# Kernel tuning notes

Measured on AMD Instinct MI355X. Metric: run time of the kernel, lower is better.

## Reference

```python
import jax, jax.numpy as jnp
import numpy as np

B, S, D, H, DK, F = 4, 2048, 1024, 16, 64, 4096


def layer_norm(x, g, b, eps=1e-5):
    mu = jnp.mean(x, axis=-1, keepdims=True)
    var = jnp.var(x, axis=-1, keepdims=True)
    return (x - mu) * jax.lax.rsqrt(var + eps) * g + b


def setup_inputs() -> dict:
    key = jax.random.key(0)
    ks = jax.random.split(key, 16)
    s = 0.02
    return {
        "src": jax.random.normal(ks[0], (B, S, D), jnp.float32),
        # per-head q/k/v projections stacked over heads: (H, D, DK)
        "Wq": jax.random.normal(ks[1], (H, D, DK), jnp.float32) * s,
        "bq": jnp.zeros((H, DK), jnp.float32),
        "Wk": jax.random.normal(ks[2], (H, D, DK), jnp.float32) * s,
        "bk": jnp.zeros((H, DK), jnp.float32),
        "Wv": jax.random.normal(ks[3], (H, D, DK), jnp.float32) * s,
        "bv": jnp.zeros((H, DK), jnp.float32),
        "Wo": jax.random.normal(ks[4], (H * DK, D), jnp.float32) * s,
        "bo": jnp.zeros((D,), jnp.float32),
        "ln1_g": jnp.ones((D,), jnp.float32),
        "ln1_b": jnp.zeros((D,), jnp.float32),
        "W1": jax.random.normal(ks[5], (D, F), jnp.float32) * s,
        "b1": jnp.zeros((F,), jnp.float32),
        "W2": jax.random.normal(ks[6], (F, D), jnp.float32) * s,
        "b2": jnp.zeros((D,), jnp.float32),
        "ln2_g": jnp.ones((D,), jnp.float32),
        "ln2_b": jnp.zeros((D,), jnp.float32),
    }


def reference(src, Wq, bq, Wk, bk, Wv, bv, Wo, bo, ln1_g, ln1_b, W1, b1, W2, b2, ln2_g, ln2_b):
    # --- multi-head attention (all heads batched via einsum) ---
    q = jnp.einsum("bsd,hdk->bhsk", src, Wq) + bq[None, :, None, :]
    k = jnp.einsum("bsd,hdk->bhsk", src, Wk) + bk[None, :, None, :]
    v = jnp.einsum("bsd,hdk->bhsk", src, Wv) + bv[None, :, None, :]
    scale = jnp.sqrt(jnp.asarray(DK, q.dtype))
    scores = jnp.einsum("bhqk,bhsk->bhqs", q, k) / scale  # [B,H,S,S]
    p = jax.nn.softmax(scores, axis=-1)
    ctx = jnp.einsum("bhqs,bhsk->bhqk", p, v)             # [B,H,S,DK]
    ctx = ctx.transpose(0, 2, 1, 3).reshape(src.shape[0], src.shape[1], H * DK)
    attn_out = ctx @ Wo + bo
    x = layer_norm(src + attn_out, ln1_g, ln1_b)
    # --- feed-forward ---
    ff = jax.nn.relu(x @ W1 + b1) @ W2 + b2
    return layer_norm(x + ff, ln2_g, ln2_b)
```

## Files before the change

### kernel.cpp

```cpp
#include <hip/hip_runtime.h>
#include <hip/hip_bf16.h>
#include <cstddef>
#include <cstdint>

typedef __bf16 bf16;
typedef __bf16 bf16x4 __attribute__((ext_vector_type(4)));
typedef __bf16 bf16x8 __attribute__((ext_vector_type(8)));
typedef float f32x4 __attribute__((ext_vector_type(4)));
typedef float f32x16 __attribute__((ext_vector_type(16)));
typedef unsigned int u32x4 __attribute__((ext_vector_type(4)));

#define GLD_LDS16(g, l) __builtin_amdgcn_global_load_lds( \
    (const __attribute__((address_space(1))) void*)(g),   \
    (__attribute__((address_space(3))) void*)(l), 16, 0, 0)

static __device__ inline unsigned int cvtpk(float lo, float hi) {
  unsigned int r;
  asm("v_cvt_pk_bf16_f32 %0, %1, %2" : "=v"(r) : "v"(lo), "v"(hi));
  return r;
}
static __device__ inline void plswap(unsigned int& a, unsigned int& b) {
  asm("v_permlane32_swap_b32 %0, %1" : "+v"(a), "+v"(b));
}
static __device__ inline float fexp2(float x) {
#if __has_builtin(__builtin_amdgcn_exp2f)
  return __builtin_amdgcn_exp2f(x);
#else
  float r; asm("v_exp_f32 %0, %1" : "=v"(r) : "v"(x)); return r;
#endif
}
static __device__ inline float tsum16(const float* e) {
  float s0 = e[0] + e[1], s1 = e[2] + e[3], s2 = e[4] + e[5], s3 = e[6] + e[7];
  float s4 = e[8] + e[9], s5 = e[10] + e[11], s6 = e[12] + e[13], s7 = e[14] + e[15];
  return ((s0 + s1) + (s2 + s3)) + ((s4 + s5) + (s6 + s7));
}

__global__ void __launch_bounds__(256)
k_cast(const float* __restrict__ in, bf16* __restrict__ out) {
  int gid = blockIdx.x * 256 + threadIdx.x;
  f32x4 a = ((const f32x4*)in)[gid * 2];
  f32x4 b = ((const f32x4*)in)[gid * 2 + 1];
  bf16x8 o;
#pragma unroll
  for (int i = 0; i < 4; ++i) { o[i] = (bf16)a[i]; o[i + 4] = (bf16)b[i]; }
  ((bf16x8*)out)[gid] = o;
}

__global__ void __launch_bounds__(256)
k_transpose_t(const float* __restrict__ in, bf16* __restrict__ out, int R, int C) {
  __shared__ float tile[64][68];
  const int nct = C >> 6;
  const int bc = blockIdx.x % nct, br = blockIdx.x / nct;
  const int r0 = br << 6, c0 = bc << 6;
  const int t = threadIdx.x;
  const int tr = t >> 4, tc4 = (t & 15) << 2;
#pragma unroll
  for (int i = 0; i < 4; ++i)
    *(f32x4*)&tile[i * 16 + tr][tc4] =
        *(const f32x4*)&in[(size_t)(r0 + i * 16 + tr) * C + c0 + tc4];
  __syncthreads();
  const int c = t >> 2, rch = (t & 3) << 4;
  bf16 ob[16];
#pragma unroll
  for (int j = 0; j < 16; ++j) ob[j] = (bf16)tile[rch + j][c];
  bf16* dst = out + (size_t)(c0 + c) * R + r0 + rch;
  *(bf16x8*)&dst[0] = *(bf16x8*)&ob[0];
  *(bf16x8*)&dst[8] = *(bf16x8*)&ob[8];
}

__global__ void __launch_bounds__(256)
k_reorder_qkv_t(const float* __restrict__ Wq, const float* __restrict__ Wk,
                const float* __restrict__ Wv, bf16* __restrict__ WqkvT) {
  __shared__ float tile[64][68];
  const int bid = blockIdx.x;
  const int sub = bid >> 4, tl = bid & 15;
  const int proj = sub >> 4, h = sub & 15;
  const float* W = (proj == 0) ? Wq : (proj == 1) ? Wk : Wv;
  const float* src = W + (size_t)h * 65536;
  const int r0 = tl << 6;
  const int t = threadIdx.x, tr = t >> 4, tc4 = (t & 15) << 2;
#pragma unroll
  for (int i = 0; i < 4; ++i)
    *(f32x4*)&tile[i * 16 + tr][tc4] =
        *(const f32x4*)&src[(size_t)(r0 + i * 16 + tr) * 64 + tc4];
  __syncthreads();
  const int c = t >> 2, rch = (t & 3) << 4;
  bf16 ob[16];
#pragma unroll
  for (int j = 0; j < 16; ++j) ob[j] = (bf16)tile[rch + j][c];
  bf16* dst = WqkvT + ((size_t)(proj * 1024 + h * 64 + c)) * 1024 + r0 + rch;
  *(bf16x8*)&dst[0] = *(bf16x8*)&ob[0];
  *(bf16x8*)&dst[8] = *(bf16x8*)&ob[8];
}

__global__ void __launch_bounds__(256)
k_bias_qkv(const float* __restrict__ bq, const float* __restrict__ bk,
           const float* __restrict__ bv, float* __restrict__ bqkv) {
  int n = blockIdx.x * 256 + threadIdx.x;
  int proj = n >> 10, wi = n & 1023;
  const float* bb = (proj == 0) ? bq : (proj == 1) ? bk : bv;
  bqkv[n] = bb[wi];
}

template <int MODE>
__global__ void __launch_bounds__(256)
k_gemm_bt(const bf16* __restrict__ A, const bf16* __restrict__ Bt,
          const float* __restrict__ bias, void* __restrict__ outp,
          int M, int N, int K,
          bf16* __restrict__ qb, bf16* __restrict__ kb, bf16* __restrict__ vb) {
  __shared__ __align__(16) bf16 As[2][128][32];
  __shared__ __align__(16) bf16 Bs[2][128][32];
  const int tid = threadIdx.x;
  const int wave = tid >> 6, lane = tid & 63;
  const int l16 = lane & 15, lq = lane >> 4;
  const int mtiles = M >> 7;
  const int tile_m = (blockIdx.x % mtiles) << 7;
  const int tile_n = (blockIdx.x / mtiles) << 7;
  const int wm = (wave >> 1) << 6, wn = (wave & 1) << 6;

  const bf16* Arow = A + (size_t)tile_m * K;
  const bf16* Brow = Bt + (size_t)tile_n * K;
  bf16* As_f = &As[0][0][0];
  bf16* Bs_f = &Bs[0][0][0];

  int gA[4], rA[4], kA[4];
#pragma unroll
  for (int j = 0; j < 4; ++j) {
    gA[j] = j * 4 + wave;
    rA[j] = (gA[j] & 7) * 16 + (lane >> 2);
    kA[j] = (gA[j] >> 3) * 32 + (lane & 3) * 8;
  }

  f32x4 acc[4][4] = {};

  for (int k0 = 0; k0 < K; k0 += 64) {
    __syncthreads();
#pragma unroll
    for (int j = 0; j < 4; ++j) {
      GLD_LDS16(Arow + (size_t)rA[j] * K + k0 + kA[j], As_f + gA[j] * 512);
      GLD_LDS16(Brow + (size_t)rA[j] * K + k0 + kA[j], Bs_f + gA[j] * 512);
    }
    __syncthreads();
#pragma unroll
    for (int p = 0; p < 2; ++p) {
      bf16x8 af[4], bfr[4];
#pragma unroll
      for (int mi = 0; mi < 4; ++mi)
        af[mi] = *(const bf16x8*)&As[p][wm + mi * 16 + l16][lq * 8];
#pragma unroll
      for (int ni = 0; ni < 4; ++ni)
        bfr[ni] = *(const bf16x8*)&Bs[p][wn + ni * 16 + l16][lq * 8];
#pragma unroll
      for (int mi = 0; mi < 4; ++mi)
#pragma unroll
        for (int ni = 0; ni < 4; ++ni)
          acc[mi][ni] = __builtin_amdgcn_mfma_f32_16x16x32_bf16(af[mi], bfr[ni], acc[mi][ni], 0, 0, 0);
    }
  }

#pragma unroll
  for (int mi = 0; mi < 4; ++mi) {
#pragma unroll
    for (int ni = 0; ni < 4; ++ni) {
      const int gn = tile_n + wn + ni * 16 + l16;
      const float bb = bias[gn];
      f32x4 v = acc[mi][ni];
      const int gm0 = tile_m + wm + mi * 16 + lq * 4;
      if (MODE == 0) {
        int proj = gn >> 10, wi = gn & 1023;
        int h = wi >> 6, dk = wi & 63;
        int b = gm0 >> 11, sdx = gm0 & 2047;
        size_t bhs = (size_t)((b << 4) + h);
        if (proj == 0) {
#pragma unroll
          for (int i = 0; i < 4; ++i)
            qb[(bhs * 2048 + sdx + i) * 64 + dk] = (bf16)((v[i] + bb) * 0.18033688f);
        } else if (proj == 1) {
#pragma unroll
          for (int i = 0; i < 4; ++i)
            kb[(bhs * 2048 + sdx + i) * 64 + dk] = (bf16)(v[i] + bb);
        } else {
          bf16x4 pk;
#pragma unroll
          for (int i = 0; i < 4; ++i) pk[i] = (bf16)(v[i] + bb);
          *(bf16x4*)&vb[(bhs * 64 + dk) * 2048 + sdx] = pk;
        }
      } else if (MODE == 1) {
#pragma unroll
        for (int i = 0; i < 4; ++i)
          ((bf16*)outp)[(size_t)(gm0 + i) * N + gn] = (bf16)(v[i] + bb);
      } else {
#pragma unroll
        for (int i = 0; i < 4; ++i)
          ((bf16*)outp)[(size_t)(gm0 + i) * N + gn] = (bf16)fmaxf(v[i] + bb, 0.f);
      }
    }
  }
}

__global__ void __launch_bounds__(256, 2)
k_attn(const bf16* __restrict__ qb, const bf16* __restrict__ kb,
       const bf16* __restrict__ vb, bf16* __restrict__ ctx) {
  __shared__ __align__(16) bf16 KsL[3][4096];
  __shared__ __align__(16) bf16 VsL[3][4096];

  const int bid = blockIdx.x;
  const int wg = (bid & 7) * 64 + (bid >> 3);
  const int bh = wg >> 3, qt = wg & 7;

  const bf16* Qp  = qb + (size_t)bh * 131072 + (size_t)qt * 16384;
  const bf16* Kbh = kb + (size_t)bh * 131072;
  const bf16* Vbh = vb + (size_t)bh * 131072;

  const int tid = threadIdx.x, wave = tid >> 6, lane = tid & 63;
  const int l31 = lane & 31, hi = lane >> 5;

  bf16x8 qfA[4], qfB[4];
  {
    const bf16* qra = Qp + (size_t)(wave * 64 + l31) * 64 + hi * 8;
    const bf16* qrb = qra + 32 * 64;
#pragma unroll
    for (int kd = 0; kd < 4; ++kd) {
      qfA[kd] = *(const bf16x8*)(qra + kd * 16);
      qfB[kd] = *(const bf16x8*)(qrb + kd * 16);
    }
  }

  const int c0 = tid, c1 = tid + 256;
  const int sw0 = ((c0 ^ (c0 >> 3)) & 7) * 8, rw0 = c0 >> 3;
  const int sw1 = ((c1 ^ (c1 >> 3)) & 7) * 8, rw1 = c1 >> 3;
  const int kof0 = rw0 * 64 + sw0, kof1 = rw1 * 64 + sw1;
  const int vof0 = rw0 * 2048 + sw0, vof1 = rw1 * 2048 + sw1;

  const int xr = (hi << 4) ^ ((l31 & 7) << 4);
  const int rb = l31 * 128 + xr;

  f32x16 oA[2] = {}, oB[2] = {};
  float lA = 0.f, lB = 0.f;

#define STAGE_KV(buf, s0)                                             \
  do {                                                                \
    GLD_LDS16(Kbh + (size_t)(s0) * 64 + kof0, &KsL[buf][c0 * 8]);     \
    GLD_LDS16(Kbh + (size_t)(s0) * 64 + kof1, &KsL[buf][c1 * 8]);     \
    GLD_LDS16(Vbh + (s0) + vof0, &VsL[buf][c0 * 8]);                  \
    GLD_LDS16(Vbh + (s0) + vof1, &VsL[buf][c1 * 8]);                  \
  } while (0)

  STAGE_KV(0, 0);
  STAGE_KV(1, 64);

  int cur = 0;
  for (int kt = 0; kt < 32; ++kt) {
    __builtin_amdgcn_sched_barrier(0);
    if (kt == 31) { asm volatile("s_waitcnt vmcnt(0)" ::: "memory"); }
    else          { asm volatile("s_waitcnt vmcnt(4)" ::: "memory"); }
    __builtin_amdgcn_s_barrier();
    __builtin_amdgcn_sched_barrier(0);

    if (kt < 30) {
      int nx = cur + 2; if (nx >= 3) nx -= 3;
      STAGE_KV(nx, (kt + 2) * 64);
    }

    const char* Kc = (const char*)&KsL[cur][0];
    const char* Vc = (const char*)&VsL[cur][0];

    bf16x8 paA[4], paB[4];
#pragma unroll
    for (int st = 0; st < 2; ++st) {
      f32x16 sA = {}, sB = {};
      __builtin_amdgcn_s_setprio(1);
#pragma unroll
      for (int kd = 0; kd < 4; ++kd) {
        bf16x8 a = *(const bf16x8*)(Kc + st * 4096 + (rb ^ (kd << 5)));
        sA = __builtin_amdgcn_mfma_f32_32x32x16_bf16(a, qfA[kd], sA, 0, 0, 0);
        sB = __builtin_amdgcn_mfma_f32_32x32x16_bf16(a, qfB[kd], sB, 0, 0, 0);
      }
      __builtin_amdgcn_s_setprio(0);

      float eA[16], eB[16];
#pragma unroll
      for (int i = 0; i < 16; ++i) {
        eA[i] = fexp2(sA[i]);
        eB[i] = fexp2(sB[i]);
      }
      lA += tsum16(eA);
      lB += tsum16(eB);
      unsigned int qdA[4][2], qdB[4][2];
#pragma unroll
      for (int g = 0; g < 4; ++g)
#pragma unroll
        for (int w = 0; w < 2; ++w) {
          qdA[g][w] = cvtpk(eA[g * 4 + w * 2], eA[g * 4 + w * 2 + 1]);
          qdB[g][w] = cvtpk(eB[g * 4 + w * 2], eB[g * 4 + w * 2 + 1]);
        }
#pragma unroll
      for (int a2 = 0; a2 < 2; ++a2) {
        unsigned int x0 = qdA[2 * a2][0], y0 = qdA[2 * a2 + 1][0];
        unsigned int x1 = qdA[2 * a2][1], y1 = qdA[2 * a2 + 1][1];
        plswap(x0, y0); plswap(x1, y1);
        u32x4 fA = {x0, x1, y0, y1};
        paA[st * 2 + a2] = __builtin_bit_cast(bf16x8, fA);
        unsigned int u0 = qdB[2 * a2][0], v0 = qdB[2 * a2 + 1][0];
        unsigned int u1 = qdB[2 * a2][1], v1 = qdB[2 * a2 + 1][1];
        plswap(u0, v0); plswap(u1, v1);
        u32x4 fB = {u0, u1, v0, v1};
        paB[st * 2 + a2] = __builtin_bit_cast(bf16x8, fB);
      }
    }

    __builtin_amdgcn_s_setprio(1);
#pragma unroll
    for (int nd = 0; nd < 2; ++nd)
#pragma unroll
      for (int ks = 0; ks < 4; ++ks) {
        bf16x8 vf = *(const bf16x8*)(Vc + nd * 4096 + (rb ^ (ks << 5)));
        oA[nd] = __builtin_amdgcn_mfma_f32_32x32x16_bf16(paA[ks], vf, oA[nd], 0, 0, 0);
        oB[nd] = __builtin_amdgcn_mfma_f32_32x32x16_bf16(paB[ks], vf, oB[nd], 0, 0, 0);
      }
    __builtin_amdgcn_s_setprio(0);

    if (++cur == 3) cur = 0;
  }
#undef STAGE_KV

  const float ltA = lA + __shfl_xor(lA, 32);
  const float ltB = lB + __shfl_xor(lB, 32);
  const float ivA = 1.f / ltA;
  const float ivB = 1.f / ltB;

  const int b = bh >> 4, h = bh & 15;
  const size_t rowbase = (size_t)(b * 2048 + qt * 256 + wave * 64);
#pragma unroll
  for (int r = 0; r < 16; ++r) {
    const int qr = (r & 3) + 8 * (r >> 2) + 4 * hi;
    const float dA = __shfl(ivA, qr);
    const float dB = __shfl(ivB, qr);
#pragma unroll
    for (int nd = 0; nd < 2; ++nd) {
      const int dk = nd * 32 + l31;
      ctx[(rowbase + qr) * 1024 + h * 64 + dk]      = (bf16)(oA[nd][r] * dA);
      ctx[(rowbase + 32 + qr) * 1024 + h * 64 + dk] = (bf16)(oB[nd][r] * dB);
    }
  }
}

template <typename RT, typename DT, typename OT>
__global__ void __launch_bounds__(256)
k_ln(const RT* __restrict__ resid, const DT* __restrict__ delta,
     const float* __restrict__ g, const float* __restrict__ bta,
     OT* __restrict__ out) {
  const int row = blockIdx.x, tid = threadIdx.x;
  const int wave = tid >> 6, lane = tid & 63;
  __shared__ float rs_[4], rs2_[4];
  const RT* r = resid + (size_t)row * 1024;
  const DT* d = delta + (size_t)row * 1024;
  OT* o = out + (size_t)row * 1024;
  float x[4], s = 0.f, s2 = 0.f;
#pragma unroll
  for (int j = 0; j < 4; ++j) {
    int idx = tid + j * 256;
    float v = (float)r[idx] + (float)d[idx];
    x[j] = v; s += v; s2 += v * v;
  }
#pragma unroll
  for (int m = 32; m >= 1; m >>= 1) { s += __shfl_xor(s, m); s2 += __shfl_xor(s2, m); }
  if (lane == 0) { rs_[wave] = s; rs2_[wave] = s2; }
  __syncthreads();
  float ts = rs_[0] + rs_[1] + rs_[2] + rs_[3];
  float ts2 = rs2_[0] + rs2_[1] + rs2_[2] + rs2_[3];
  float mean = ts * (1.f / 1024.f);
  float var = ts2 * (1.f / 1024.f) - mean * mean;
  float rstd = rsqrtf(var + 1e-5f);
#pragma unroll
  for (int j = 0; j < 4; ++j) {
    int idx = tid + j * 256;
    o[idx] = (OT)((x[j] - mean) * rstd * g[idx] + bta[idx]);
  }
}

extern "C" void kernel_launch(void* const* d_in, const int* in_sizes, int n_in,
                              void* d_out, int out_size, void* d_ws, size_t ws_size,
                              hipStream_t stream) {
  const float* src  = (const float*)d_in[0];
  const float* Wq   = (const float*)d_in[1];
  const float* bq   = (const float*)d_in[2];
  const float* Wk   = (const float*)d_in[3];
  const float* bk   = (const float*)d_in[4];
  const float* Wv   = (const float*)d_in[5];
  const float* bv   = (const float*)d_in[6];
  const float* Wo   = (const float*)d_in[7];
  const float* bo   = (const float*)d_in[8];
  const float* ln1g = (const float*)d_in[9];
  const float* ln1b = (const float*)d_in[10];
  const float* W1   = (const float*)d_in[11];
  const float* b1   = (const float*)d_in[12];
  const float* W2   = (const float*)d_in[13];
  const float* b2   = (const float*)d_in[14];
  const float* ln2g = (const float*)d_in[15];
  const float* ln2b = (const float*)d_in[16];

  char* p = (char*)d_ws;
  bf16*  WqkvT = (bf16*)p;  p += (size_t)3072 * 1024 * 2;
  float* bqkv  = (float*)p; p += 16384;
  bf16*  WoT   = (bf16*)p;  p += (size_t)1024 * 1024 * 2;
  bf16*  W1T   = (bf16*)p;  p += (size_t)4096 * 1024 * 2;
  bf16*  W2T   = (bf16*)p;  p += (size_t)1024 * 4096 * 2;
  bf16*  srcb  = (bf16*)p;  p += (size_t)8388608 * 2;
  bf16*  qbuf  = (bf16*)p;  p += (size_t)8388608 * 2;
  bf16*  kbuf  = (bf16*)p;  p += (size_t)8388608 * 2;
  bf16*  vbuf  = (bf16*)p;  p += (size_t)8388608 * 2;
  bf16*  ctx   = (bf16*)p;  p += (size_t)8388608 * 2;
  bf16*  x1    = (bf16*)p;  p += (size_t)8388608 * 2;
  bf16*  ff1   = (bf16*)p;  p += (size_t)8192 * 4096 * 2;
  bf16*  tmp   = qbuf;

  k_cast<<<4096, 256, 0, stream>>>(src, srcb);
  k_reorder_qkv_t<<<768, 256, 0, stream>>>(Wq, Wk, Wv, WqkvT);
  k_bias_qkv<<<12, 256, 0, stream>>>(bq, bk, bv, bqkv);
  k_transpose_t<<<256, 256, 0, stream>>>(Wo, WoT, 1024, 1024);
  k_transpose_t<<<1024, 256, 0, stream>>>(W1, W1T, 1024, 4096);
  k_transpose_t<<<1024, 256, 0, stream>>>(W2, W2T, 4096, 1024);

  k_gemm_bt<0><<<64 * 24, 256, 0, stream>>>(srcb, WqkvT, bqkv, nullptr,
                                            8192, 3072, 1024, qbuf, kbuf, vbuf);
  k_attn<<<512, 256, 0, stream>>>(qbuf, kbuf, vbuf, ctx);
  k_gemm_bt<1><<<64 * 8, 256, 0, stream>>>(ctx, WoT, bo, tmp,
                                           8192, 1024, 1024, nullptr, nullptr, nullptr);
  k_ln<float, bf16, bf16><<<8192, 256, 0, stream>>>(src, tmp, ln1g, ln1b, x1);
  k_gemm_bt<2><<<64 * 32, 256, 0, stream>>>(x1, W1T, b1, ff1,
                                            8192, 4096, 1024, nullptr, nullptr, nullptr);
  k_gemm_bt<1><<<64 * 8, 256, 0, stream>>>(ff1, W2T, b2, tmp,
                                           8192, 1024, 4096, nullptr, nullptr, nullptr);
  k_ln<bf16, bf16, float><<<8192, 256, 0, stream>>>(x1, tmp, ln2g, ln2b, (float*)d_out);
}
```

Before: 513.9 us.

## Replace GEMM with 8-wave 256-row tiled kernel using swizzled LDS pipeline

Replaces the 128x128 four-wave GEMM with a 512-thread kernel that computes 256-row tiles (128 or 256 columns) split into quadrant sub-tiles. It uses a four-slot LDS ring with XOR-swizzled columns, interleaves global-to-LDS staging with MFMA phases under explicit barriers, vmcnt waits and setprio, and remaps block IDs in groups of eight. The goal is more operand reuse per LDS load, fewer LDS bank conflicts, and latency hiding for all four projection and FFN GEMMs. In exchange it runs one workgroup per CU with heavy register use, and correctness depends on the hand-tuned wait counts and tile divisibility.

```diff
diff --git a/kernel.cpp b/kernel.cpp
--- a/kernel.cpp
+++ b/kernel.cpp
@@ -13,6 +13,9 @@
 #define GLD_LDS16(g, l) __builtin_amdgcn_global_load_lds( \
     (const __attribute__((address_space(1))) void*)(g),   \
     (__attribute__((address_space(3))) void*)(l), 16, 0, 0)
+
+#define SBAR __builtin_amdgcn_s_barrier()
+#define SCHED0 __builtin_amdgcn_sched_barrier(0)
 
 static __device__ inline unsigned int cvtpk(float lo, float hi) {
   unsigned int r;
@@ -102,100 +105,172 @@
   bqkv[n] = bb[wi];
 }
 
-template <int MODE>
-__global__ void __launch_bounds__(256)
-k_gemm_bt(const bf16* __restrict__ A, const bf16* __restrict__ Bt,
-          const float* __restrict__ bias, void* __restrict__ outp,
-          int M, int N, int K,
-          bf16* __restrict__ qb, bf16* __restrict__ kb, bf16* __restrict__ vb) {
-  __shared__ __align__(16) bf16 As[2][128][32];
-  __shared__ __align__(16) bf16 Bs[2][128][32];
+template <int MODE, int NREP>
+__global__ void __launch_bounds__(512, 1)
+k_gemm8(const bf16* __restrict__ A, const bf16* __restrict__ Bt,
+        const float* __restrict__ bias, void* __restrict__ outp,
+        int M, int N, int K,
+        bf16* __restrict__ qb, bf16* __restrict__ kb, bf16* __restrict__ vb) {
+  constexpr int BN = 128 * NREP;
+  constexpr int BROWS = 64 * NREP;
+  __shared__ __align__(16) bf16 Asl[4][8192];
+  __shared__ __align__(16) bf16 Bsl[4][BROWS * 64];
+
   const int tid = threadIdx.x;
-  const int wave = tid >> 6, lane = tid & 63;
+  const int lane = tid & 63, wave = tid >> 6;
   const int l16 = lane & 15, lq = lane >> 4;
-  const int mtiles = M >> 7;
-  const int tile_m = (blockIdx.x % mtiles) << 7;
-  const int tile_n = (blockIdx.x / mtiles) << 7;
-  const int wm = (wave >> 1) << 6, wn = (wave & 1) << 6;
-
-  const bf16* Arow = A + (size_t)tile_m * K;
-  const bf16* Brow = Bt + (size_t)tile_n * K;
-  bf16* As_f = &As[0][0][0];
-  bf16* Bs_f = &Bs[0][0][0];
-
-  int gA[4], rA[4], kA[4];
-#pragma unroll
-  for (int j = 0; j < 4; ++j) {
-    gA[j] = j * 4 + wave;
-    rA[j] = (gA[j] & 7) * 16 + (lane >> 2);
-    kA[j] = (gA[j] >> 3) * 32 + (lane & 3) * 8;
-  }
-
-  f32x4 acc[4][4] = {};
-
-  for (int k0 = 0; k0 < K; k0 += 64) {
-    __syncthreads();
-#pragma unroll
-    for (int j = 0; j < 4; ++j) {
-      GLD_LDS16(Arow + (size_t)rA[j] * K + k0 + kA[j], As_f + gA[j] * 512);
-      GLD_LDS16(Brow + (size_t)rA[j] * K + k0 + kA[j], Bs_f + gA[j] * 512);
-    }
-    __syncthreads();
-#pragma unroll
-    for (int p = 0; p < 2; ++p) {
-      bf16x8 af[4], bfr[4];
+  const int qwm = wave >> 2, qwn = wave & 3;
+
+  const int mtiles = M >> 8;
+  const int nwg = gridDim.x, cpx = nwg >> 3;
+  const int wg = (blockIdx.x & 7) * cpx + (blockIdx.x >> 3);
+  const int tile_m = (wg % mtiles) << 8;
+  const int tile_n = (wg / mtiles) * BN;
+
+  const bf16* Abase = A + (size_t)tile_m * K;
+  const bf16* Bbase = Bt + (size_t)tile_n * K;
+
+  const int crow = tid >> 3;
+  const int ccol = ((tid & 7) ^ (crow & 7)) << 3;
+
+  auto stageA = [&](int T, int h, int slot) {
+    const bf16* s_ = Abase + (size_t)(h * 128 + crow) * K + T * 64 + ccol;
+    GLD_LDS16(s_, &Asl[slot][tid * 8]);
+    GLD_LDS16(s_ + (size_t)64 * K, &Asl[slot][tid * 8 + 4096]);
+  };
+  auto stageB = [&](int T, int h, int slot) {
+    const bf16* s_ = Bbase + (size_t)(h * BROWS + crow) * K + T * 64 + ccol;
+    GLD_LDS16(s_, &Bsl[slot][tid * 8]);
+    if (NREP == 2) GLD_LDS16(s_ + (size_t)64 * K, &Bsl[slot][tid * 8 + 4096]);
+  };
+
+  const int xk = l16 & 7;
+  const int swz0 = (lq ^ xk) * 16;
+  const int swz1 = ((4 | lq) ^ xk) * 16;
+  const int arow_b = (qwm * 64 + l16) * 128;
+  const int brow_b = (qwn * 16 * NREP + l16) * 128;
+
+  bf16x8 af[4][2];
+  bf16x8 bb[2][NREP][2];
+  f32x4 acc[2][2][4][NREP] = {};
+
+  auto dsA = [&](int slot) {
+    const char* Ab = (const char*)&Asl[slot][0] + arow_b;
+#pragma unroll
+    for (int mi = 0; mi < 4; ++mi) {
+      af[mi][0] = *(const bf16x8*)(Ab + mi * 2048 + swz0);
+      af[mi][1] = *(const bf16x8*)(Ab + mi * 2048 + swz1);
+    }
+  };
+  auto dsB = [&](int slot, int h) {
+    const char* Bb = (const char*)&Bsl[slot][0] + brow_b;
+#pragma unroll
+    for (int ni = 0; ni < NREP; ++ni) {
+      bb[h][ni][0] = *(const bf16x8*)(Bb + ni * 2048 + swz0);
+      bb[h][ni][1] = *(const bf16x8*)(Bb + ni * 2048 + swz1);
+    }
+  };
+
+#define MF(mh, nh)                                                           \
+  {                                                                          \
+    __builtin_amdgcn_s_setprio(1);                                           \
+    _Pragma("unroll") for (int mi = 0; mi < 4; ++mi)                         \
+        _Pragma("unroll") for (int ni = 0; ni < NREP; ++ni)                  \
+        _Pragma("unroll") for (int p = 0; p < 2; ++p)                        \
+            acc[mh][nh][mi][ni] = __builtin_amdgcn_mfma_f32_16x16x32_bf16(   \
+                af[mi][p], bb[nh][ni][p], acc[mh][nh][mi][ni], 0, 0, 0);     \
+    __builtin_amdgcn_s_setprio(0);                                           \
+  }
+#define VMW(n) asm volatile("s_waitcnt vmcnt(" #n ")" ::: "memory")
+
+  const int NT = K >> 6;
+  const int NI = NT >> 1;
+
+  stageA(0, 0, 0); stageA(0, 1, 1); stageB(0, 0, 0); stageB(0, 1, 1);
+  stageA(1, 0, 2); stageB(1, 0, 2); stageB(1, 1, 3);
+  SCHED0;
+  if (NREP == 2) { VMW(6); } else { VMW(4); }
+  SBAR;
+
+  for (int i = 0; i < NI; ++i) {
+    const int t2 = 2 * i + 2, t3 = 2 * i + 3;
+    const bool tv = (t2 < NT);
+    const bool last = (i == NI - 1);
+    dsA(0); dsB(0, 0);
+    stageA(2 * i + 1, 1, 3);
+    SBAR; MF(0, 0); SBAR;
+    dsB(1, 1);
+    if (tv) stageA(t2, 0, 0);
+    SBAR; MF(0, 1); SBAR;
+    dsA(1);
+    if (tv) stageB(t2, 0, 0);
+    SBAR; MF(1, 0); SBAR;
+    if (tv) stageB(t2, 1, 1);
+    SCHED0;
+    if (last) { VMW(0); }
+    else if (NREP == 2) { VMW(6); }
+    else { VMW(4); }
+    SBAR; MF(1, 1); SBAR;
+    dsA(2); dsB(2, 0);
+    if (tv) stageA(t2, 1, 1);
+    SBAR; MF(0, 0); SBAR;
+    dsB(3, 1);
+    if (tv) stageA(t3, 0, 2);
+    SBAR; MF(0, 1); SBAR;
+    dsA(3);
+    if (tv) stageB(t3, 0, 2);
+    SBAR; MF(1, 0); SBAR;
+    if (tv) stageB(t3, 1, 3);
+    if (!last) {
+      SCHED0;
+      if (NREP == 2) { VMW(6); } else { VMW(4); }
+    }
+    SBAR; MF(1, 1); SBAR;
+  }
+#undef MF
+#undef VMW
+
+#pragma unroll
+  for (int mh = 0; mh < 2; ++mh)
+#pragma unroll
+    for (int nh = 0; nh < 2; ++nh)
 #pragma unroll
       for (int mi = 0; mi < 4; ++mi)
-        af[mi] = *(const bf16x8*)&As[p][wm + mi * 16 + l16][lq * 8];
-#pragma unroll
-      for (int ni = 0; ni < 4; ++ni)
-        bfr[ni] = *(const bf16x8*)&Bs[p][wn + ni * 16 + l16][lq * 8];
-#pragma unroll
-      for (int mi = 0; mi < 4; ++mi)
-#pragma unroll
-        for (int ni = 0; ni < 4; ++ni)
-          acc[mi][ni] = __builtin_amdgcn_mfma_f32_16x16x32_bf16(af[mi], bfr[ni], acc[mi][ni], 0, 0, 0);
-    }
-  }
-
-#pragma unroll
-  for (int mi = 0; mi < 4; ++mi) {
-#pragma unroll
-    for (int ni = 0; ni < 4; ++ni) {
-      const int gn = tile_n + wn + ni * 16 + l16;
-      const float bb = bias[gn];
-      f32x4 v = acc[mi][ni];
-      const int gm0 = tile_m + wm + mi * 16 + lq * 4;
-      if (MODE == 0) {
-        int proj = gn >> 10, wi = gn & 1023;
-        int h = wi >> 6, dk = wi & 63;
-        int b = gm0 >> 11, sdx = gm0 & 2047;
-        size_t bhs = (size_t)((b << 4) + h);
-        if (proj == 0) {
-#pragma unroll
-          for (int i = 0; i < 4; ++i)
-            qb[(bhs * 2048 + sdx + i) * 64 + dk] = (bf16)((v[i] + bb) * 0.18033688f);
-        } else if (proj == 1) {
-#pragma unroll
-          for (int i = 0; i < 4; ++i)
-            kb[(bhs * 2048 + sdx + i) * 64 + dk] = (bf16)(v[i] + bb);
-        } else {
-          bf16x4 pk;
-#pragma unroll
-          for (int i = 0; i < 4; ++i) pk[i] = (bf16)(v[i] + bb);
-          *(bf16x4*)&vb[(bhs * 64 + dk) * 2048 + sdx] = pk;
+#pragma unroll
+        for (int ni = 0; ni < NREP; ++ni) {
+          const int gn = tile_n + nh * (BN / 2) + qwn * 16 * NREP + ni * 16 + l16;
+          const float bv = bias[gn];
+          f32x4 v = acc[mh][nh][mi][ni];
+          const int gm0 = tile_m + mh * 128 + qwm * 64 + mi * 16 + lq * 4;
+          if (MODE == 0) {
+            int proj = gn >> 10, wi = gn & 1023;
+            int h = wi >> 6, dk = wi & 63;
+            int b = gm0 >> 11, sdx = gm0 & 2047;
+            size_t bhs = (size_t)((b << 4) + h);
+            if (proj == 0) {
+#pragma unroll
+              for (int i2 = 0; i2 < 4; ++i2)
+                qb[(bhs * 2048 + sdx + i2) * 64 + dk] = (bf16)((v[i2] + bv) * 0.18033688f);
+            } else if (proj == 1) {
+#pragma unroll
+              for (int i2 = 0; i2 < 4; ++i2)
+                kb[(bhs * 2048 + sdx + i2) * 64 + dk] = (bf16)(v[i2] + bv);
+            } else {
+              bf16x4 pk;
+#pragma unroll
+              for (int i2 = 0; i2 < 4; ++i2) pk[i2] = (bf16)(v[i2] + bv);
+              *(bf16x4*)&vb[(bhs * 64 + dk) * 2048 + sdx] = pk;
+            }
+          } else if (MODE == 1) {
+#pragma unroll
+            for (int i2 = 0; i2 < 4; ++i2)
+              ((bf16*)outp)[(size_t)(gm0 + i2) * N + gn] = (bf16)(v[i2] + bv);
+          } else {
+#pragma unroll
+            for (int i2 = 0; i2 < 4; ++i2)
+              ((bf16*)outp)[(size_t)(gm0 + i2) * N + gn] = (bf16)fmaxf(v[i2] + bv, 0.f);
+          }
         }
-      } else if (MODE == 1) {
-#pragma unroll
-        for (int i = 0; i < 4; ++i)
-          ((bf16*)outp)[(size_t)(gm0 + i) * N + gn] = (bf16)(v[i] + bb);
-      } else {
-#pragma unroll
-        for (int i = 0; i < 4; ++i)
-          ((bf16*)outp)[(size_t)(gm0 + i) * N + gn] = (bf16)fmaxf(v[i] + bb, 0.f);
-      }
-    }
-  }
 }
 
 __global__ void __launch_bounds__(256, 2)
@@ -251,11 +326,11 @@
 
   int cur = 0;
   for (int kt = 0; kt < 32; ++kt) {
-    __builtin_amdgcn_sched_barrier(0);
+    SCHED0;
     if (kt == 31) { asm volatile("s_waitcnt vmcnt(0)" ::: "memory"); }
     else          { asm volatile("s_waitcnt vmcnt(4)" ::: "memory"); }
     __builtin_amdgcn_s_barrier();
-    __builtin_amdgcn_sched_barrier(0);
+    SCHED0;
 
     if (kt < 30) {
       int nx = cur + 2; if (nx >= 3) nx -= 3;
@@ -422,15 +497,15 @@
   k_transpose_t<<<1024, 256, 0, stream>>>(W1, W1T, 1024, 4096);
   k_transpose_t<<<1024, 256, 0, stream>>>(W2, W2T, 4096, 1024);
 
-  k_gemm_bt<0><<<64 * 24, 256, 0, stream>>>(srcb, WqkvT, bqkv, nullptr,
-                                            8192, 3072, 1024, qbuf, kbuf, vbuf);
+  k_gemm8<0, 1><<<768, 512, 0, stream>>>(srcb, WqkvT, bqkv, nullptr,
+                                         8192, 3072, 1024, qbuf, kbuf, vbuf);
   k_attn<<<512, 256, 0, stream>>>(qbuf, kbuf, vbuf, ctx);
-  k_gemm_bt<1><<<64 * 8, 256, 0, stream>>>(ctx, WoT, bo, tmp,
-                                           8192, 1024, 1024, nullptr, nullptr, nullptr);
+  k_gemm8<1, 1><<<256, 512, 0, stream>>>(ctx, WoT, bo, tmp,
+                                         8192, 1024, 1024, nullptr, nullptr, nullptr);
   k_ln<float, bf16, bf16><<<8192, 256, 0, stream>>>(src, tmp, ln1g, ln1b, x1);
-  k_gemm_bt<2><<<64 * 32, 256, 0, stream>>>(x1, W1T, b1, ff1,
-                                            8192, 4096, 1024, nullptr, nullptr, nullptr);
-  k_gemm_bt<1><<<64 * 8, 256, 0, stream>>>(ff1, W2T, b2, tmp,
-                                           8192, 1024, 4096, nullptr, nullptr, nullptr);
+  k_gemm8<2, 2><<<512, 512, 0, stream>>>(x1, W1T, b1, ff1,
+                                         8192, 4096, 1024, nullptr, nullptr, nullptr);
+  k_gemm8<1, 1><<<256, 512, 0, stream>>>(ff1, W2T, b2, tmp,
+                                         8192, 1024, 4096, nullptr, nullptr, nullptr);
   k_ln<bf16, bf16, float><<<8192, 256, 0, stream>>>(x1, tmp, ln2g, ln2b, (float*)d_out);
 }
```

Result: slower. 525.2 us (+2.2%).
